# Optimization experiments

Measured on AMD Instinct MI355X. Metric: run time of the kernel, lower is better.

## Reference

```python
import jax, jax.numpy as jnp
import numpy as np

MATSIZE = 1024
TRIU_LEN = MATSIZE * (MATSIZE + 1) // 2  # 524800
_rows, _cols = np.triu_indices(MATSIZE)
ROWS = jnp.asarray(_rows)
COLS = jnp.asarray(_cols)


def setup_inputs() -> dict:
    key = jax.random.key(0)
    inputs = jax.random.normal(key, (128, TRIU_LEN), dtype=jnp.float32)
    return {"inputs": inputs}


def reference(inputs) -> jnp.ndarray:
    # Scatter each batch vector into the upper triangle of an (M, M) matrix,
    # zeros elsewhere. Vectorized over the batch via a single indexed set.
    B = inputs.shape[0]
    out = jnp.zeros((B, MATSIZE, MATSIZE), dtype=inputs.dtype)
    return out.at[:, ROWS, COLS].set(inputs)
```

## Files before the change

### kernel.cpp

```cpp
#include <hip/hip_runtime.h>


constexpr int M = 1024;
constexpr int BATCH = 128;
constexpr int TRIU_LEN = M * (M + 1) / 2;
constexpr int QUADS_PER_ROW = M / 4;

__global__ __launch_bounds__(256) void triu_scatter_kernel(
    const float* __restrict__ in, float* __restrict__ out) {
    int tid = blockIdx.x * blockDim.x + threadIdx.x;
    int qc = tid & (QUADS_PER_ROW - 1);
    int r  = (tid >> 8) & (M - 1);
    int b  = tid >> 18;
    int c0 = qc << 2;

    int row_base = r * M - (r * (r - 1)) / 2 - r;
    const float* inb = in + (long)b * TRIU_LEN + row_base;

    float4 v;
    if (c0 >= r) {
        v.x = inb[c0];
        v.y = inb[c0 + 1];
        v.z = inb[c0 + 2];
        v.w = inb[c0 + 3];
    } else if (c0 + 3 < r) {
        v = make_float4(0.f, 0.f, 0.f, 0.f);
    } else {
        v.x = (c0     >= r) ? inb[c0]     : 0.f;
        v.y = (c0 + 1 >= r) ? inb[c0 + 1] : 0.f;
        v.z = (c0 + 2 >= r) ? inb[c0 + 2] : 0.f;
        v.w = (c0 + 3 >= r) ? inb[c0 + 3] : 0.f;
    }

    reinterpret_cast<float4*>(out)[tid] = v;
}

extern "C" void kernel_launch(void* const* d_in, const int* in_sizes, int n_in,
                              void* d_out, int out_size, void* d_ws, size_t ws_size,
                              hipStream_t stream) {
    const float* in = (const float*)d_in[0];
    float* out = (float*)d_out;

    const int total_quads = BATCH * M * QUADS_PER_ROW;
    const int block = 256;
    const int grid = total_quads / block;

    triu_scatter_kernel<<<grid, block, 0, stream>>>(in, out);
}
```

Measured before the change: 665.0 us.

## Use persistent grid-stride loop over batches with nontemporal stores

Launches a fixed grid of 2048 blocks. Each thread loops over 64 batch pairs, striding two matrices per iteration, so index math and branch decisions are hoisted out of the loop. Output writes become nontemporal stores to reduce cache pollution on this write-heavy kernel. The diagonal-boundary case uses clamped addresses so its loads are unconditional. This cuts per-element integer overhead and block scheduling cost, but lowers the number of resident waves available to hide memory latency.

```diff
diff --git a/kernel.cpp b/kernel.cpp
--- a/kernel.cpp
+++ b/kernel.cpp
@@ -4,35 +4,69 @@
 constexpr int M = 1024;
 constexpr int BATCH = 128;
 constexpr int TRIU_LEN = M * (M + 1) / 2;
-constexpr int QUADS_PER_ROW = M / 4;
+constexpr int QPR = M / 4;
+constexpr int TOTAL_QUADS = BATCH * M * QPR;
+constexpr int BLOCK = 256;
+constexpr int GRID = 2048;
+constexpr int NTHREADS = BLOCK * GRID;
+constexpr int ITERS = TOTAL_QUADS / NTHREADS;
 
-__global__ __launch_bounds__(256) void triu_scatter_kernel(
+static_assert(NTHREADS == 2 * M * QPR, "stride must be exactly 2 matrices");
+static_assert(TOTAL_QUADS % NTHREADS == 0, "exact tiling");
+
+typedef float v4f __attribute__((ext_vector_type(4)));
+
+__global__ __launch_bounds__(BLOCK) void triu_scatter_kernel(
     const float* __restrict__ in, float* __restrict__ out) {
-    int tid = blockIdx.x * blockDim.x + threadIdx.x;
-    int qc = tid & (QUADS_PER_ROW - 1);
-    int r  = (tid >> 8) & (M - 1);
-    int b  = tid >> 18;
-    int c0 = qc << 2;
+    const int tid = blockIdx.x * BLOCK + threadIdx.x;
+    const int qc = tid & (QPR - 1);
+    const int r  = (tid >> 8) & (M - 1);
+    const int b0 = tid >> 18;
+    const int c0 = qc << 2;
 
-    int row_base = r * M - (r * (r - 1)) / 2 - r;
-    const float* inb = in + (long)b * TRIU_LEN + row_base;
+    const int row_base = r * (M - 1) - ((r * (r - 1)) >> 1);
+    const float* p = in + b0 * TRIU_LEN + row_base;
+    v4f* o = reinterpret_cast<v4f*>(out) + tid;
 
-    float4 v;
     if (c0 >= r) {
-        v.x = inb[c0];
-        v.y = inb[c0 + 1];
-        v.z = inb[c0 + 2];
-        v.w = inb[c0 + 3];
+#pragma unroll 8
+        for (int k = 0; k < ITERS; ++k) {
+            v4f v;
+            v.x = p[c0];
+            v.y = p[c0 + 1];
+            v.z = p[c0 + 2];
+            v.w = p[c0 + 3];
+            __builtin_nontemporal_store(v, o);
+            p += 2 * TRIU_LEN;
+            o += NTHREADS;
+        }
     } else if (c0 + 3 < r) {
-        v = make_float4(0.f, 0.f, 0.f, 0.f);
+        const v4f z = {0.f, 0.f, 0.f, 0.f};
+#pragma unroll 8
+        for (int k = 0; k < ITERS; ++k) {
+            __builtin_nontemporal_store(z, o);
+            o += NTHREADS;
+        }
     } else {
-        v.x = (c0     >= r) ? inb[c0]     : 0.f;
-        v.y = (c0 + 1 >= r) ? inb[c0 + 1] : 0.f;
-        v.z = (c0 + 2 >= r) ? inb[c0 + 2] : 0.f;
-        v.w = (c0 + 3 >= r) ? inb[c0 + 3] : 0.f;
+        const int c1 = c0 + 1, c2 = c0 + 2, c3 = c0 + 3;
+        const bool m1 = (c1 >= r), m2 = (c2 >= r);
+        const int a1 = m1 ? c1 : c3;
+        const int a2 = m2 ? c2 : c3;
+#pragma unroll 4
+        for (int k = 0; k < ITERS; ++k) {
+            v4f v;
+            const float ly = p[a1];
+            const float lz = p[a2];
+            const float lw = p[c3];
+            v.x = 0.f;
+            v.y = m1 ? ly : 0.f;
+            v.z = m2 ? lz : 0.f;
+            v.w = lw;
+            __builtin_nontemporal_store(v, o);
+            p += 2 * TRIU_LEN;
+            o += NTHREADS;
+        }
     }
-
-    reinterpret_cast<float4*>(out)[tid] = v;
 }
 
 extern "C" void kernel_launch(void* const* d_in, const int* in_sizes, int n_in,
@@ -40,10 +74,5 @@
                               hipStream_t stream) {
     const float* in = (const float*)d_in[0];
     float* out = (float*)d_out;
-
-    const int total_quads = BATCH * M * QUADS_PER_ROW;
-    const int block = 256;
-    const int grid = total_quads / block;
-
-    triu_scatter_kernel<<<grid, block, 0, stream>>>(in, out);
+    triu_scatter_kernel<<<GRID, BLOCK, 0, stream>>>(in, out);
 }
```

Measured after the change: 742.8 us. +11.7%, slower.
